# Kernel tuning notes

Measured on AMD Instinct MI355X. Metric: run time of the kernel, lower is better.

## Reference

```python
import jax, jax.numpy as jnp
import numpy as np

N_NODES = 100000
N_EDGES = 625000
D = 128


def _sage_conv(x, edge_index, W_l, b_l, W_r):
    """PyG SAGEConv with mean aggregation.
    out_i = (mean_{j->i} x_j) @ W_l^T + b_l + x_i @ W_r^T
    edge_index[0] = source j, edge_index[1] = target i.
    """
    src, dst = edge_index[0], edge_index[1]
    msgs = x[src]  # [E, D] gather
    agg = jax.ops.segment_sum(msgs, dst, num_segments=x.shape[0])  # [N, D]
    deg = jax.ops.segment_sum(jnp.ones((msgs.shape[0],), x.dtype), dst,
                              num_segments=x.shape[0])
    agg = agg / jnp.maximum(deg, 1.0)[:, None]  # mean; isolated nodes -> 0
    return agg @ W_l.T + b_l + x @ W_r.T


def setup_inputs() -> dict:
    key = jax.random.key(0)
    ks = jax.random.split(key, 7)
    s = 1.0 / np.sqrt(D)
    x = jax.random.normal(ks[0], (N_NODES, D), dtype=jnp.float32)
    edge_index = jax.random.randint(ks[1], (2, N_EDGES), 0, N_NODES, dtype=jnp.int64)
    return {
        "x": x,
        "edge_index": edge_index,
        "W1_l": jax.random.normal(ks[2], (D, D), dtype=jnp.float32) * s,
        "b1": jnp.zeros((D,), dtype=jnp.float32),
        "W1_r": jax.random.normal(ks[3], (D, D), dtype=jnp.float32) * s,
        "W2_l": jax.random.normal(ks[4], (D, D), dtype=jnp.float32) * s,
        "b2": jnp.zeros((D,), dtype=jnp.float32),
        "W2_r": jax.random.normal(ks[5], (D, D), dtype=jnp.float32) * s,
    }


def reference(x, edge_index, W1_l, b1, W1_r, W2_l, b2, W2_r):
    h = jax.nn.relu(_sage_conv(x, edge_index, W1_l, b1, W1_r))
    out = _sage_conv(h, edge_index, W2_l, b2, W2_r)
    return out
```

## Files before the change

kernel.cpp:

```cpp
#include <hip/hip_runtime.h>
#include <hip/hip_bf16.h>


#define D 128
#define SCAN_BLK 1024

typedef __attribute__((ext_vector_type(8))) short bf16x8;
typedef __attribute__((ext_vector_type(4))) float f32x4;

__device__ inline ushort f2bf(float f) {
    uint u = __float_as_uint(f);
    u += 0x7FFF + ((u >> 16) & 1);
    return (ushort)(u >> 16);
}
__device__ inline float bf2f(ushort h) { return __uint_as_float(((uint)h) << 16); }


__global__ void count_deg(const int* __restrict__ ei, int* __restrict__ deg, int E) {
    int e = blockIdx.x * 256 + threadIdx.x;
    if (e < E) atomicAdd(&deg[ei[E + e]], 1);
}

__global__ __launch_bounds__(SCAN_BLK) void scan_local(
        const int* __restrict__ deg, int* __restrict__ rowptr,
        int* __restrict__ partials, int n) {
    __shared__ int sdata[SCAN_BLK];
    int tid = threadIdx.x;
    int i = blockIdx.x * SCAN_BLK + tid;
    int v = (i < n) ? deg[i] : 0;
    sdata[tid] = v;
    __syncthreads();
    #pragma unroll
    for (int off = 1; off < SCAN_BLK; off <<= 1) {
        int t = (tid >= off) ? sdata[tid - off] : 0;
        __syncthreads();
        sdata[tid] += t;
        __syncthreads();
    }
    if (i < n) rowptr[i] = sdata[tid] - v;
    if (tid == SCAN_BLK - 1) partials[blockIdx.x] = sdata[SCAN_BLK - 1];
}

__global__ __launch_bounds__(SCAN_BLK) void scan_partials(
        const int* __restrict__ partials, int* __restrict__ bases,
        int* __restrict__ rowptr, int nblocks, int n) {
    __shared__ int sdata[SCAN_BLK];
    int tid = threadIdx.x;
    int v = (tid < nblocks) ? partials[tid] : 0;
    sdata[tid] = v;
    __syncthreads();
    #pragma unroll
    for (int off = 1; off < SCAN_BLK; off <<= 1) {
        int t = (tid >= off) ? sdata[tid - off] : 0;
        __syncthreads();
        sdata[tid] += t;
        __syncthreads();
    }
    if (tid < nblocks) bases[tid] = sdata[tid] - v;
    if (tid == SCAN_BLK - 1) rowptr[n] = sdata[SCAN_BLK - 1];
}

__global__ void add_bases(int* __restrict__ rowptr, const int* __restrict__ bases, int n) {
    int i = blockIdx.x * 256 + threadIdx.x;
    if (i < n) rowptr[i] += bases[i >> 10];
}

__global__ void fill_csr(const int* __restrict__ ei, int* __restrict__ cursor,
                         const int* __restrict__ rowptr, int* __restrict__ csr, int E) {
    int e = blockIdx.x * 256 + threadIdx.x;
    if (e < E) {
        int s = ei[e];
        int d = ei[E + e];
        int pos = atomicAdd(&cursor[d], 1);
        csr[rowptr[d] + pos] = s;
    }
}


__global__ __launch_bounds__(256) void to_bf16(const float* __restrict__ in,
                                               ushort* __restrict__ out, int n8) {
    int i = blockIdx.x * 256 + threadIdx.x;
    if (i >= n8) return;
    const float4* p = (const float4*)in;
    float4 a = p[i * 2], b = p[i * 2 + 1];
    uint4 pk;
    pk.x = (uint)f2bf(a.x) | ((uint)f2bf(a.y) << 16);
    pk.y = (uint)f2bf(a.z) | ((uint)f2bf(a.w) << 16);
    pk.z = (uint)f2bf(b.x) | ((uint)f2bf(b.y) << 16);
    pk.w = (uint)f2bf(b.z) | ((uint)f2bf(b.w) << 16);
    *(uint4*)&out[i * 8] = pk;
}


__global__ __launch_bounds__(256) void prep_w(const float* __restrict__ Wl,
                                              const float* __restrict__ Wr,
                                              ushort* __restrict__ wcat) {
    int t = blockIdx.x * 256 + threadIdx.x;
    int e = t * 4;
    int row = e >> 8;
    int k = e & 255;
    const float* src = (k < 128) ? &Wl[row * 128 + k] : &Wr[row * 128 + k - 128];
    float4 v = *(const float4*)src;
    uint2 pk;
    pk.x = (uint)f2bf(v.x) | ((uint)f2bf(v.y) << 16);
    pk.y = (uint)f2bf(v.z) | ((uint)f2bf(v.w) << 16);
    *(uint2*)&wcat[e] = pk;
}


__global__ __launch_bounds__(256) void agg_mean_b(
        const ushort* __restrict__ feat, const int* __restrict__ rowptr,
        const int* __restrict__ csr, ushort* __restrict__ aggout, int n) {
    int node = (blockIdx.x * 256 + threadIdx.x) >> 5;
    int lane = threadIdx.x & 31;
    if (node >= n) return;
    int beg = rowptr[node], end = rowptr[node + 1];
    float a0 = 0.f, a1 = 0.f, a2 = 0.f, a3 = 0.f;
    for (int e = beg; e < end; ++e) {
        int s = csr[e];
        uint2 v = *(const uint2*)&feat[s * D + lane * 4];
        a0 += __uint_as_float(v.x << 16);
        a1 += __uint_as_float(v.x & 0xFFFF0000u);
        a2 += __uint_as_float(v.y << 16);
        a3 += __uint_as_float(v.y & 0xFFFF0000u);
    }
    float inv = (end > beg) ? 1.0f / (float)(end - beg) : 0.0f;
    uint2 pk;
    pk.x = (uint)f2bf(a0 * inv) | ((uint)f2bf(a1 * inv) << 16);
    pk.y = (uint)f2bf(a2 * inv) | ((uint)f2bf(a3 * inv) << 16);
    *(uint2*)&aggout[node * D + lane * 4] = pk;
}


template <bool OUT_BF16, bool RELU>
__global__ __launch_bounds__(256) void sage_gemm_mfma(
        const ushort* __restrict__ aggb, const ushort* __restrict__ featb,
        const ushort* __restrict__ wcat, const float* __restrict__ bias,
        void* __restrict__ outp, int n) {
    __shared__ char lds[65536];
    int tid = threadIdx.x;

    #pragma unroll
    for (int i = 0; i < 16; ++i) {
        int e = (tid + i * 256) * 8;
        int byte = e * 2;
        int row = byte >> 9;
        int sb = byte ^ ((row & 7) << 4);
        *(uint4*)&lds[sb] = *(const uint4*)&wcat[e];
    }
    __syncthreads();

    int wave = tid >> 6, l = tid & 63;
    int l15 = l & 15, lhi = l >> 4;
    int row_base = blockIdx.x * 128 + wave * 32;

    f32x4 zero = {0.f, 0.f, 0.f, 0.f};
    f32x4 acc[2][8];
    #pragma unroll
    for (int t = 0; t < 2; ++t)
        #pragma unroll
        for (int j = 0; j < 8; ++j) acc[t][j] = zero;

    int ra0 = row_base + l15;       if (ra0 > n - 1) ra0 = n - 1;
    int ra1 = row_base + 16 + l15;  if (ra1 > n - 1) ra1 = n - 1;

    for (int kc = 0; kc < 8; ++kc) {
        const ushort* asrc = (kc < 4) ? aggb : featb;
        int klocal = (kc & 3) * 32 + lhi * 8;
        bf16x8 a0 = *(const bf16x8*)&asrc[ra0 * D + klocal];
        bf16x8 a1 = *(const bf16x8*)&asrc[ra1 * D + klocal];
        bf16x8 b[8];
        #pragma unroll
        for (int j = 0; j < 8; ++j) {
            int brow = l15 + j * 16;
            int bbyte = (brow << 9) + kc * 64 + lhi * 16;
            b[j] = *(const bf16x8*)&lds[bbyte ^ ((brow & 7) << 4)];
        }
        #pragma unroll
        for (int j = 0; j < 8; ++j) {
            acc[0][j] = __builtin_amdgcn_mfma_f32_16x16x32_bf16(a0, b[j], acc[0][j], 0, 0, 0);
            acc[1][j] = __builtin_amdgcn_mfma_f32_16x16x32_bf16(a1, b[j], acc[1][j], 0, 0, 0);
        }
    }

    #pragma unroll
    for (int t = 0; t < 2; ++t) {
        #pragma unroll
        for (int j = 0; j < 8; ++j) {
            int col = j * 16 + l15;
            float bv = bias[col];
            #pragma unroll
            for (int r = 0; r < 4; ++r) {
                int grow = row_base + t * 16 + lhi * 4 + r;
                if (grow >= n) continue;
                float v = acc[t][j][r] + bv;
                if (RELU) v = fmaxf(v, 0.f);
                if (OUT_BF16) ((ushort*)outp)[grow * D + col] = f2bf(v);
                else          ((float*)outp)[grow * D + col] = v;
            }
        }
    }
}


extern "C" void kernel_launch(void* const* d_in, const int* in_sizes, int n_in,
                              void* d_out, int out_size, void* d_ws, size_t ws_size,
                              hipStream_t stream) {
    const float* x   = (const float*)d_in[0];
    const int*   ei  = (const int*)d_in[1];
    const float* W1l = (const float*)d_in[2];
    const float* b1  = (const float*)d_in[3];
    const float* W1r = (const float*)d_in[4];
    const float* W2l = (const float*)d_in[5];
    const float* b2  = (const float*)d_in[6];
    const float* W2r = (const float*)d_in[7];
    float* out = (float*)d_out;

    const int N = in_sizes[0] / D;
    const int E = in_sizes[1] / 2;

    ushort* aggb  = (ushort*)d_ws;
    ushort* hb    = aggb + (size_t)N * D;
    ushort* wcat  = hb + (size_t)N * D;
    int* deg      = (int*)(wcat + 128 * 256);
    int* rowptr   = deg + N;
    int* csr      = rowptr + N + 1;
    int* parts    = csr + E;
    int* bases    = parts + SCAN_BLK;

    const int nchunks = (N + SCAN_BLK - 1) / SCAN_BLK;
    const int eblk = (E + 255) / 256;
    const int nblk = (N + 255) / 256;
    const int n8 = N * D / 8;

    hipMemsetAsync(deg, 0, (size_t)N * sizeof(int), stream);
    count_deg<<<eblk, 256, 0, stream>>>(ei, deg, E);
    scan_local<<<nchunks, SCAN_BLK, 0, stream>>>(deg, rowptr, parts, N);
    scan_partials<<<1, SCAN_BLK, 0, stream>>>(parts, bases, rowptr, nchunks, N);
    add_bases<<<nblk, 256, 0, stream>>>(rowptr, bases, N);
    hipMemsetAsync(deg, 0, (size_t)N * sizeof(int), stream);
    fill_csr<<<eblk, 256, 0, stream>>>(ei, deg, rowptr, csr, E);

    to_bf16<<<(n8 + 255) / 256, 256, 0, stream>>>(x, hb, n8);

    const int aggblk = (N * 32 + 255) / 256;
    const int gemmblk = (N + 127) / 128;

    prep_w<<<32, 256, 0, stream>>>(W1l, W1r, wcat);
    agg_mean_b<<<aggblk, 256, 0, stream>>>(hb, rowptr, csr, aggb, N);
    sage_gemm_mfma<true, true><<<gemmblk, 256, 0, stream>>>(aggb, hb, wcat, b1, hb, N);

    prep_w<<<32, 256, 0, stream>>>(W2l, W2r, wcat);
    agg_mean_b<<<aggblk, 256, 0, stream>>>(hb, rowptr, csr, aggb, N);
    sage_gemm_mfma<false, false><<<gemmblk, 256, 0, stream>>>(aggb, hb, wcat, b2, out, N);
}
```

Before: 328.3 us.

## Unroll edge gather by eight and halve GEMM LDS footprint

The mean-aggregation loop now issues eight independent feature gathers per iteration, masking out-of-range edges with zero weights, to raise memory-level parallelism on the irregular gather. The GEMM kernel loads the concatenated weight matrix into shared memory in two 32 KB halves instead of one 64 KB block, allowing more resident blocks per CU. The cost is an extra barrier and a reload between halves. Masked lanes in the gather still perform redundant loads.

```diff
diff --git a/kernel.cpp b/kernel.cpp
--- a/kernel.cpp
+++ b/kernel.cpp
@@ -13,7 +13,6 @@
     u += 0x7FFF + ((u >> 16) & 1);
     return (ushort)(u >> 16);
 }
-__device__ inline float bf2f(ushort h) { return __uint_as_float(((uint)h) << 16); }
 
 
 __global__ void count_deg(const int* __restrict__ ei, int* __restrict__ deg, int E) {
@@ -116,13 +115,24 @@
     if (node >= n) return;
     int beg = rowptr[node], end = rowptr[node + 1];
     float a0 = 0.f, a1 = 0.f, a2 = 0.f, a3 = 0.f;
-    for (int e = beg; e < end; ++e) {
-        int s = csr[e];
-        uint2 v = *(const uint2*)&feat[s * D + lane * 4];
-        a0 += __uint_as_float(v.x << 16);
-        a1 += __uint_as_float(v.x & 0xFFFF0000u);
-        a2 += __uint_as_float(v.y << 16);
-        a3 += __uint_as_float(v.y & 0xFFFF0000u);
+    for (int e = beg; e < end; e += 8) {
+        uint2 v[8];
+        float w[8];
+        #pragma unroll
+        for (int u = 0; u < 8; ++u) {
+            int idx = e + u;
+            int safe = (idx < end) ? idx : beg;
+            int s = csr[safe];
+            v[u] = *(const uint2*)&feat[s * D + lane * 4];
+            w[u] = (idx < end) ? 1.f : 0.f;
+        }
+        #pragma unroll
+        for (int u = 0; u < 8; ++u) {
+            a0 = fmaf(w[u], __uint_as_float(v[u].x << 16), a0);
+            a1 = fmaf(w[u], __uint_as_float(v[u].x & 0xFFFF0000u), a1);
+            a2 = fmaf(w[u], __uint_as_float(v[u].y << 16), a2);
+            a3 = fmaf(w[u], __uint_as_float(v[u].y & 0xFFFF0000u), a3);
+        }
     }
     float inv = (end > beg) ? 1.0f / (float)(end - beg) : 0.0f;
     uint2 pk;
@@ -137,19 +147,8 @@
         const ushort* __restrict__ aggb, const ushort* __restrict__ featb,
         const ushort* __restrict__ wcat, const float* __restrict__ bias,
         void* __restrict__ outp, int n) {
-    __shared__ char lds[65536];
+    __shared__ char lds[32768];
     int tid = threadIdx.x;
-
-    #pragma unroll
-    for (int i = 0; i < 16; ++i) {
-        int e = (tid + i * 256) * 8;
-        int byte = e * 2;
-        int row = byte >> 9;
-        int sb = byte ^ ((row & 7) << 4);
-        *(uint4*)&lds[sb] = *(const uint4*)&wcat[e];
-    }
-    __syncthreads();
-
     int wave = tid >> 6, l = tid & 63;
     int l15 = l & 15, lhi = l >> 4;
     int row_base = blockIdx.x * 128 + wave * 32;
@@ -164,22 +163,34 @@
     int ra0 = row_base + l15;       if (ra0 > n - 1) ra0 = n - 1;
     int ra1 = row_base + 16 + l15;  if (ra1 > n - 1) ra1 = n - 1;
 
-    for (int kc = 0; kc < 8; ++kc) {
-        const ushort* asrc = (kc < 4) ? aggb : featb;
-        int klocal = (kc & 3) * 32 + lhi * 8;
-        bf16x8 a0 = *(const bf16x8*)&asrc[ra0 * D + klocal];
-        bf16x8 a1 = *(const bf16x8*)&asrc[ra1 * D + klocal];
-        bf16x8 b[8];
-        #pragma unroll
-        for (int j = 0; j < 8; ++j) {
-            int brow = l15 + j * 16;
-            int bbyte = (brow << 9) + kc * 64 + lhi * 16;
-            b[j] = *(const bf16x8*)&lds[bbyte ^ ((brow & 7) << 4)];
-        }
-        #pragma unroll
-        for (int j = 0; j < 8; ++j) {
-            acc[0][j] = __builtin_amdgcn_mfma_f32_16x16x32_bf16(a0, b[j], acc[0][j], 0, 0, 0);
-            acc[1][j] = __builtin_amdgcn_mfma_f32_16x16x32_bf16(a1, b[j], acc[1][j], 0, 0, 0);
+    #pragma unroll
+    for (int half = 0; half < 2; ++half) {
+        if (half) __syncthreads();
+        #pragma unroll
+        for (int rep = 0; rep < 8; ++rep) {
+            int chunk = tid + rep * 256;
+            int r = chunk >> 4;
+            int c = chunk & 15;
+            int byte = (r << 8) + (c << 4);
+            int sb = byte ^ ((r & 7) << 4);
+            *(uint4*)&lds[sb] = *(const uint4*)&wcat[r * 256 + half * 128 + c * 8];
+        }
+        __syncthreads();
+
+        const ushort* asrc = half ? featb : aggb;
+        #pragma unroll
+        for (int kc = 0; kc < 4; ++kc) {
+            int klocal = kc * 32 + lhi * 8;
+            bf16x8 a0 = *(const bf16x8*)&asrc[ra0 * D + klocal];
+            bf16x8 a1 = *(const bf16x8*)&asrc[ra1 * D + klocal];
+            #pragma unroll
+            for (int j = 0; j < 8; ++j) {
+                int brow = l15 + j * 16;
+                int bbyte = (brow << 8) + kc * 64 + lhi * 16;
+                bf16x8 b = *(const bf16x8*)&lds[bbyte ^ ((brow & 7) << 4)];
+                acc[0][j] = __builtin_amdgcn_mfma_f32_16x16x32_bf16(a0, b, acc[0][j], 0, 0, 0);
+                acc[1][j] = __builtin_amdgcn_mfma_f32_16x16x32_bf16(a1, b, acc[1][j], 0, 0, 0);
+            }
         }
     }
 
```

Result: faster. 290.5 us (-11.5%).
